# Optimization experiments

Measured on AMD Instinct MI355X. Metric: run time of the kernel, lower is better.

## Reference

```python
import jax, jax.numpy as jnp
import numpy as np
from jax import lax
from jax.scipy.linalg import solve_triangular

SR = 16000
FRAME_PERIOD = 80
FFT_LENGTH = 1024
WIN_MS = 30
EPS = 1e-05
DEFAULT_F0 = 150.0
B, T, N = 8, 320000, 4000

N_BAND = int(np.log2(SR / 600))  # 4
CUTOFF = [SR / 2 ** i for i in range(2, N_BAND + 1)]
CUTOFF.append(CUTOFF[-1])  # [4000, 2000, 1000, 1000]
SEG = [int(c * WIN_MS / 500 + 1.5) for c in CUTOFF]  # [241, 121, 61, 61]

_HHP_VALS = [0.00041447996898231424, 0.0007812505141729248, -0.0010917236836275842,
             -0.001986792567596759, 0.0020903896961562292, 0.004094057027284935,
             -0.0034025808529816698, -0.007496154127205602, 0.004972263339933064,
             0.012738791249119802, -0.006696032689574911, -0.020694051570247052,
             0.008432436565041345, 0.03307438375870053, -0.010018936738799522,
             -0.05423136140580825, 0.011293988915051487, 0.10020081367388213,
             -0.012120546202484579, -0.316300210390957, 0.5124068258062764]
_HLP_VALS = [-0.0006548817007748305, 7.561994958159384e-05, 0.0020408456937895227,
             -0.0007468053532203044, -0.004350223568826493, 0.0025966428382642732,
             0.007639602282756696, -0.006490411890149785, -0.011765804538954506,
             0.013649908479276255, 0.01636866479016021, -0.026075976030529347,
             -0.020910294856659444, 0.04826072503231665, 0.02476784661104811,
             -0.09617846758336064, -0.027359756709866623, 0.3148805216163004,
             0.5282734359405503]

def _qmf_high():
    h = np.zeros(41)
    h[:21] = _HHP_VALS
    h[21:] = h[19::-1]
    return h.astype(np.float32)

def _qmf_low():
    h = np.zeros(37)
    h[:19] = _HLP_VALS
    h[19:] = h[17::-1]
    return h.astype(np.float32)

def _make_window():
    w = np.zeros((N_BAND, SEG[0]), np.float32)
    for i, s in enumerate(SEG):
        w[i, :s] = np.hanning(s + 2)[1:-1]
    return w

def _interp_tables():
    coarse = np.concatenate([[0.0], [SR / 2 ** i for i in range(N_BAND, 0, -1)]])
    freq = np.arange(FFT_LENGTH // 2 + 1) * (SR / FFT_LENGTH)
    idx = np.clip(np.searchsorted(coarse, freq) - 1, 0, len(coarse) - 2)
    x0 = coarse[:-1]
    dx = coarse[1:] - x0
    wts = ((freq - x0[idx]) / dx[idx]).astype(np.float32)
    return idx.astype(np.int32), wts

_HHP = _qmf_high()
_HLP = _qmf_low()
_WIN = _make_window()
_IDX, _WTS = _interp_tables()


def _qmf_conv(x, h):
    # x: (B, T), h: (k,). Reflection pad k//2, cross-correlation, stride 2.
    p = h.shape[0] // 2
    xp = jnp.pad(x, ((0, 0), (p, p)), mode='reflect')
    out = lax.conv_general_dilated(xp[:, None, :], h[None, None, :], (2,), 'VALID',
                                   dimension_numbers=('NCH', 'OIH', 'NCH'))
    return out[:, 0, :]


def setup_inputs() -> dict:
    key = jax.random.key(0)
    k1, k2 = jax.random.split(key)
    x = jax.random.normal(k1, (B, T), jnp.float32)
    f0 = 100.0 + 200.0 * jax.random.uniform(k2, (B, N), jnp.float32)  # 100-300 Hz
    return {"x": x, "f0": f0}


def reference(x, f0):
    hHP = jnp.asarray(_HHP)
    hLP = jnp.asarray(_HLP)
    f0 = lax.stop_gradient(jnp.where(f0 <= 32, DEFAULT_F0, f0))
    Bn, Nf = f0.shape
    time_axis = jnp.arange(Nf, dtype=f0.dtype) * (FRAME_PERIOD / SR)
    bidx = jnp.arange(Bn)[:, None, None]
    eye6 = EPS * jnp.eye(6, dtype=x.dtype)
    lx = x
    bap = []
    for i in range(N_BAND):
        if i < N_BAND - 1:
            hx = _qmf_conv(lx, hHP)
            lx = _qmf_conv(lx, hLP)
            xb = hx
        else:
            xb = lx
        seg = SEG[i]
        tmp_fs = 2.0 * CUTOFF[i]
        pitch = tmp_fs / f0
        t0 = (pitch + 0.5).astype(jnp.int32)
        index_bias = (pitch * 0.5 + 0.5).astype(jnp.int32)
        curr_pos = (time_axis * tmp_fs + 1.5).astype(jnp.int32)[None, :]
        origin = curr_pos - index_bias  # (B, N)
        j = jnp.arange(-1, seg + 1)  # (seg+2,)
        T1 = xb.shape[-1] - 1
        ia = jnp.clip((origin - t0)[..., None] + j, 0, T1)
        ib = jnp.clip((origin + t0)[..., None] + j, 0, T1)
        Ha = xb[bidx, ia]  # (B, N, seg+2)
        Hb = xb[bidx, ib]

        def unfold3(a):  # size-3 sliding windows -> (B, N, seg, 3)
            return jnp.stack([a[..., 0:seg], a[..., 1:seg + 1], a[..., 2:seg + 2]], axis=-1)

        H = jnp.concatenate([unfold3(Ha), unfold3(Hb)], axis=-1)  # (B, N, seg, 6)
        w = jnp.asarray(_WIN[i, :seg])
        Hw = jnp.swapaxes(H, -2, -1) * w  # (B, N, 6, seg)
        R = Hw @ H  # (B, N, 6, 6)
        ig = jnp.clip(origin[..., None] + j[1:-1], 0, T1)
        X = xb[bidx, ig][..., None]  # (B, N, seg, 1)
        L = jnp.linalg.cholesky(R + eye6)
        b = Hw @ X  # (B, N, 6, 1)
        y1 = solve_triangular(L, b, lower=True)
        a = solve_triangular(jnp.swapaxes(L, -2, -1), y1, lower=False)
        HaX = H @ a  # (B, N, seg, 1)
        wsqrt = jnp.sqrt(w)
        wx = wsqrt * X[..., 0]
        wxHa = wsqrt * (X - HaX)[..., 0]
        A = jnp.std(wxHa, axis=-1, ddof=1) / (jnp.std(wx, axis=-1, ddof=1) + 1e-16)
        bap.append(A)
    bap.append(bap[-1])
    ap = jnp.stack(bap[::-1], axis=-1)  # (B, N, n_band+1), low->high freq
    # piecewise-linear interpolation in log domain onto fft bins
    y = jnp.log(ap)
    y0 = y[..., :-1]
    dy = y[..., 1:] - y0
    yi = jnp.take(dy, jnp.asarray(_IDX), axis=-1) * jnp.asarray(_WTS) \
         + jnp.take(y0, jnp.asarray(_IDX), axis=-1)
    return jnp.exp(yi)  # (B, N, fft//2+1)
```

## Files before the change

### kernel.cpp

```cpp
#include <hip/hip_runtime.h>
#include <math.h>

#define NB 8
#define NF 4000
#define NFRAMES (NB * NF)
#define TOTF (4 * NFRAMES)

__constant__ float c_hhp[21] = {
    0.00041447996898231424, 0.0007812505141729248, -0.0010917236836275842,
    -0.001986792567596759,  0.0020903896961562292, 0.004094057027284935,
    -0.0034025808529816698, -0.007496154127205602, 0.004972263339933064,
    0.012738791249119802,   -0.006696032689574911, -0.020694051570247052,
    0.008432436565041345,   0.03307438375870053,   -0.010018936738799522,
    -0.05423136140580825,   0.011293988915051487,  0.10020081367388213,
    -0.012120546202484579,  -0.316300210390957,    0.5124068258062764};
__constant__ float c_hlp[19] = {
    -0.0006548817007748305, 7.561994958159384e-05, 0.0020408456937895227,
    -0.0007468053532203044, -0.004350223568826493, 0.0025966428382642732,
    0.007639602282756696,   -0.006490411890149785, -0.011765804538954506,
    0.013649908479276255,   0.01636866479016021,   -0.026075976030529347,
    -0.020910294856659444,  0.04826072503231665,   0.02476784661104811,
    -0.09617846758336064,   -0.027359756709866623, 0.3148805216163004,
    0.5282734359405503};

__device__ __forceinline__ int reflidx(int i, int len) {
  if (i < 0) i = -i;
  if (i >= len) i = 2 * len - 2 - i;
  return i;
}
__device__ __forceinline__ int clampi(int i, int hi) {
  return min(max(i, 0), hi);
}
__device__ __forceinline__ float4 ld4(const float* p) {
  return *reinterpret_cast<const float4*>(p);
}
__device__ __forceinline__ void st4(float* p, float4 v) {
  *reinterpret_cast<float4*>(p) = v;
}

__global__ __launch_bounds__(256) void qmf_kernel(
    const float* __restrict__ in, int len, float* __restrict__ outH,
    float* __restrict__ outL, float2* __restrict__ wtab) {
  int half = len >> 1;
  int gid = blockIdx.x * 256 + threadIdx.x;
  if (gid >= NB * half) {
    if (wtab) {
      const int segs[4] = {241, 121, 61, 61};
      int k = threadIdx.x;
      for (int i = 0; i < 4; ++i) {
        float v = 0.f;
        if (k < segs[i]) {
          double ang = 2.0 * 3.14159265358979323846 * (double)(k + 1) /
                       (double)(segs[i] + 1);
          v = (float)(0.5 - 0.5 * cos(ang));
        }
        wtab[i * 256 + k] = make_float2(v, sqrtf(v));
      }
    }
    return;
  }
  int b = gid / half;
  int nn = gid - b * half;
  const float* row = in + (size_t)b * len;
  int c = 2 * nn;
  float sh = 0.f, sl = 0.f;
  if (c >= 20 && c <= len - 22) {
    const float2* p2 = reinterpret_cast<const float2*>(row + (c - 20));
    float v[42];
#pragma unroll
    for (int j = 0; j < 21; ++j) {
      float2 t = p2[j];
      v[2 * j] = t.x;
      v[2 * j + 1] = t.y;
    }
#pragma unroll
    for (int t = 0; t < 41; ++t) sh += v[t] * c_hhp[t <= 20 ? t : 40 - t];
#pragma unroll
    for (int t = 0; t < 37; ++t) sl += v[t + 2] * c_hlp[t <= 18 ? t : 36 - t];
  } else {
#pragma unroll
    for (int t = 0; t < 41; ++t)
      sh += row[reflidx(c + t - 20, len)] * c_hhp[t <= 20 ? t : 40 - t];
#pragma unroll
    for (int t = 0; t < 37; ++t)
      sl += row[reflidx(c + t - 18, len)] * c_hlp[t <= 18 ? t : 36 - t];
  }
  outH[(size_t)b * half + nn] = sh;
  outL[(size_t)b * half + nn] = sl;
}

__device__ __forceinline__ void accum1(float wk, float wsk, float h0, float h1,
                                       float h2, float h3, float h4, float h5,
                                       float x, float* __restrict__ rr,
                                       float* __restrict__ bv,
                                       float* __restrict__ gv, float& sxx,
                                       float& s1x) {
  sxx += wk * x * x;
  s1x += wsk * x;
  float wh0 = wk * h0, wh1 = wk * h1, wh2 = wk * h2, wh3 = wk * h3,
        wh4 = wk * h4, wh5 = wk * h5;
  gv[0] += wsk * h0; gv[1] += wsk * h1; gv[2] += wsk * h2;
  gv[3] += wsk * h3; gv[4] += wsk * h4; gv[5] += wsk * h5;
  bv[0] += wh0 * x;  bv[1] += wh1 * x;  bv[2] += wh2 * x;
  bv[3] += wh3 * x;  bv[4] += wh4 * x;  bv[5] += wh5 * x;
  rr[0] += wh0 * h0;  rr[1] += wh0 * h1;  rr[2] += wh0 * h2;
  rr[3] += wh0 * h3;  rr[4] += wh0 * h4;  rr[5] += wh0 * h5;
  rr[6] += wh1 * h1;  rr[7] += wh1 * h2;  rr[8] += wh1 * h3;
  rr[9] += wh1 * h4;  rr[10] += wh1 * h5; rr[11] += wh2 * h2;
  rr[12] += wh2 * h3; rr[13] += wh2 * h4; rr[14] += wh2 * h5;
  rr[15] += wh3 * h3; rr[16] += wh3 * h4; rr[17] += wh3 * h5;
  rr[18] += wh4 * h4; rr[19] += wh4 * h5; rr[20] += wh5 * h5;
}

template <int GS, int NITER, bool CLAMP>
__device__ __forceinline__ void acc_loop(
    const float* __restrict__ row, int T1, int base_a, int base_b, int origin,
    int sub, const float2* __restrict__ wtab, float rr[21], float bv[6],
    float gv[6], float& sxx, float& s1x) {
  if (!CLAMP) {
    const float* pa = row + base_a + 4 * sub;
    const float* pb = row + base_b + 4 * sub;
    const float* pg = row + origin + 4 * sub;
    const float* pw = reinterpret_cast<const float*>(wtab + 4 * sub);
#pragma unroll 2
    for (int j = 0; j < NITER; ++j) {
      const int off = j * 4 * GS;
      float4 a0 = ld4(pa + off);
      float4 a1 = ld4(pa + off + 4);
      float4 b0 = ld4(pb + off);
      float4 b1 = ld4(pb + off + 4);
      float4 xx = ld4(pg + off);
      float4 w01 = ld4(pw + 2 * off);
      float4 w23 = ld4(pw + 2 * off + 4);
      accum1(w01.x, w01.y, a0.x, a0.y, a0.z, b0.x, b0.y, b0.z, xx.x, rr, bv,
             gv, sxx, s1x);
      accum1(w01.z, w01.w, a0.y, a0.z, a0.w, b0.y, b0.z, b0.w, xx.y, rr, bv,
             gv, sxx, s1x);
      accum1(w23.x, w23.y, a0.z, a0.w, a1.x, b0.z, b0.w, b1.x, xx.z, rr, bv,
             gv, sxx, s1x);
      accum1(w23.z, w23.w, a0.w, a1.x, a1.y, b0.w, b1.x, b1.y, xx.w, rr, bv,
             gv, sxx, s1x);
    }
  } else {
#pragma unroll 2
    for (int j = 0; j < NITER; ++j) {
#pragma unroll
      for (int m = 0; m < 4; ++m) {
        int k = 4 * (sub + j * GS) + m;
        float2 wp = wtab[k];
        int ia = base_a + k, ib = base_b + k;
        float h0 = row[clampi(ia, T1)];
        float h1 = row[clampi(ia + 1, T1)];
        float h2 = row[clampi(ia + 2, T1)];
        float h3 = row[clampi(ib, T1)];
        float h4 = row[clampi(ib + 1, T1)];
        float h5 = row[clampi(ib + 2, T1)];
        float x = row[clampi(origin + k, T1)];
        accum1(wp.x, wp.y, h0, h1, h2, h3, h4, h5, x, rr, bv, gv, sxx, s1x);
      }
    }
  }
}

template <int SEG, int LGS, int NITER>
__device__ __forceinline__ void band_body(
    const float* __restrict__ xb, int bandLen, const float* __restrict__ f0,
    float tmp_fs, const float2* __restrict__ wtab, float* __restrict__ sums_col,
    int blk) {
  constexpr int GS = 1 << LGS;
  constexpr int FPB = 256 / GS;
  constexpr int KMAX = 4 * GS * NITER;
  const int tid = threadIdx.x;
  const int sub = tid & (GS - 1);
  const int frame = blk * FPB + (tid >> LGS);
  const int b = frame / NF;
  const int n = frame - b * NF;

  float f0v = f0[frame];
  if (f0v <= 32.0f) f0v = 150.0f;
  float pitch = tmp_fs / f0v;
  int t0 = (int)(__fadd_rn(pitch, 0.5f));
  int ibias = (int)(__fadd_rn(__fmul_rn(pitch, 0.5f), 0.5f));
  float tt = __fmul_rn((float)n, 0.005f);
  int curr = (int)(__fadd_rn(__fmul_rn(tt, tmp_fs), 1.5f));
  int origin = curr - ibias;
  const int T1 = bandLen - 1;
  const float* row = xb + (size_t)b * bandLen;
  const int base_a = origin - t0 - 1;
  const int base_b = origin + t0 - 1;

  float rr[21], bv[6], gv[6], sxx = 0.f, s1x = 0.f;
#pragma unroll
  for (int i = 0; i < 21; ++i) rr[i] = 0.f;
#pragma unroll
  for (int i = 0; i < 6; ++i) bv[i] = 0.f;
#pragma unroll
  for (int i = 0; i < 6; ++i) gv[i] = 0.f;

  const bool fast = (base_a >= 0) && (base_b + KMAX + 3 <= T1);
  if (fast)
    acc_loop<GS, NITER, false>(row, T1, base_a, base_b, origin, sub, wtab, rr,
                               bv, gv, sxx, s1x);
  else
    acc_loop<GS, NITER, true>(row, T1, base_a, base_b, origin, sub, wtab, rr,
                              bv, gv, sxx, s1x);

#pragma unroll
  for (int off = GS / 2; off >= 1; off >>= 1) {
#pragma unroll
    for (int i = 0; i < 21; ++i) rr[i] += __shfl_xor(rr[i], off, 64);
#pragma unroll
    for (int i = 0; i < 6; ++i) bv[i] += __shfl_xor(bv[i], off, 64);
#pragma unroll
    for (int i = 0; i < 6; ++i) gv[i] += __shfl_xor(gv[i], off, 64);
    sxx += __shfl_xor(sxx, off, 64);
    s1x += __shfl_xor(s1x, off, 64);
  }

  if (sub == 0) {
    float* sp = sums_col + frame;
#pragma unroll
    for (int i = 0; i < 21; ++i) sp[(size_t)i * TOTF] = rr[i];
#pragma unroll
    for (int i = 0; i < 6; ++i) sp[(size_t)(21 + i) * TOTF] = bv[i];
#pragma unroll
    for (int i = 0; i < 6; ++i) sp[(size_t)(27 + i) * TOTF] = gv[i];
    sp[(size_t)33 * TOTF] = sxx;
    sp[(size_t)34 * TOTF] = s1x;
  }
}

__global__ __launch_bounds__(256) void bands_kernel(
    const float* __restrict__ hx0, const float* __restrict__ hx1,
    const float* __restrict__ hx2, const float* __restrict__ lx2,
    const float* __restrict__ f0, const float2* __restrict__ wtab,
    float* __restrict__ sums) {
  int blk = blockIdx.x;
  if (blk < 2000) {
    band_body<241, 4, 4>(hx0, 160000, f0, 8000.0f, wtab + 0 * 256,
                         sums + 0 * NFRAMES, blk);
  } else if (blk < 3000) {
    band_body<121, 3, 4>(hx1, 80000, f0, 4000.0f, wtab + 1 * 256,
                         sums + 1 * NFRAMES, blk - 2000);
  } else if (blk < 3500) {
    band_body<61, 2, 4>(hx2, 40000, f0, 2000.0f, wtab + 2 * 256,
                        sums + 2 * NFRAMES, blk - 3000);
  } else {
    band_body<61, 2, 4>(lx2, 40000, f0, 2000.0f, wtab + 3 * 256,
                        sums + 3 * NFRAMES, blk - 3500);
  }
}

__global__ __launch_bounds__(256) void solve_kernel(
    const float* __restrict__ sums, float* __restrict__ Aarr) {
  const int t = blockIdx.x * 256 + threadIdx.x;
  float v[35];
#pragma unroll
  for (int i = 0; i < 35; ++i) v[i] = sums[(size_t)i * TOTF + t];
  const float nf = (t >= 2 * NFRAMES) ? 61.0f
                   : (t >= NFRAMES)   ? 121.0f
                                      : 241.0f;
  float sxx = v[33], s1x = v[34];

  float M[6][6], invd[6];
  {
    int c = 0;
#pragma unroll
    for (int p = 0; p < 6; ++p)
#pragma unroll
      for (int q = p; q < 6; ++q) {
        M[p][q] = v[c];
        M[q][p] = v[c];
        ++c;
      }
#pragma unroll
    for (int p = 0; p < 6; ++p) M[p][p] += 1e-5f;
  }
#pragma unroll
  for (int p = 0; p < 6; ++p) {
    float d = M[p][p];
#pragma unroll
    for (int j = 0; j < 6; ++j)
      if (j < p) d -= M[p][j] * M[p][j];
    d = sqrtf(d);
    M[p][p] = d;
    float inv = 1.0f / d;
    invd[p] = inv;
#pragma unroll
    for (int q = 0; q < 6; ++q)
      if (q > p) {
        float s = M[q][p];
#pragma unroll
        for (int j = 0; j < 6; ++j)
          if (j < p) s -= M[q][j] * M[p][j];
        M[q][p] = s * inv;
      }
  }
  float yv[6], av[6];
#pragma unroll
  for (int p = 0; p < 6; ++p) {
    float s = v[21 + p];
#pragma unroll
    for (int j = 0; j < 6; ++j)
      if (j < p) s -= M[p][j] * yv[j];
    yv[p] = s * invd[p];
  }
#pragma unroll
  for (int p = 5; p >= 0; --p) {
    float s = yv[p];
#pragma unroll
    for (int j = 0; j < 6; ++j)
      if (j > p) s -= M[j][p] * av[j];
    av[p] = s * invd[p];
  }

  float adotb = 0.f, adotg = 0.f, quad = 0.f;
  {
    int c = 0;
#pragma unroll
    for (int p = 0; p < 6; ++p) {
      adotb += av[p] * v[21 + p];
      adotg += av[p] * v[27 + p];
#pragma unroll
      for (int q = p; q < 6; ++q) {
        float tt = av[p] * av[q] * v[c++];
        quad += (q == p) ? tt : 2.f * tt;
      }
    }
  }
  float s2r = sxx - 2.f * adotb + quad;
  float s1r = s1x - adotg;
  float vx = (sxx - s1x * s1x / nf) / (nf - 1.0f);
  float vr = (s2r - s1r * s1r / nf) / (nf - 1.0f);
  float sx = sqrtf(fmaxf(vx, 0.f));
  float sr = sqrtf(fmaxf(vr, 0.f));
  Aarr[t] = sr / (sx + 1e-16f);
}

__global__ __launch_bounds__(256) void interp_kernel(
    const float* __restrict__ A, float* __restrict__ out) {
  const int wave = threadIdx.x >> 6;
  const int lane = threadIdx.x & 63;
  const int f = blockIdx.x * 4 + wave;
  float l0 = __logf(A[0 * NFRAMES + f]);
  float l1 = __logf(A[1 * NFRAMES + f]);
  float l2 = __logf(A[2 * NFRAMES + f]);
  float l3 = __logf(A[3 * NFRAMES + f]);
  float d1 = l2 - l3, d2 = l1 - l2, d3 = l0 - l1;
  float* orow = out + (size_t)f * 513;
  float vals[8];
#pragma unroll
  for (int m = 0; m < 8; ++m) {
    int k = 8 * lane + m;
    float y0, dy, c;
    int k0;
    if (k <= 64) {
      y0 = l3; dy = 0.f; k0 = 0; c = 0.015625f;
    } else if (k <= 128) {
      y0 = l3; dy = d1; k0 = 64; c = 0.015625f;
    } else if (k <= 256) {
      y0 = l2; dy = d2; k0 = 128; c = 0.0078125f;
    } else {
      y0 = l1; dy = d3; k0 = 256; c = 0.00390625f;
    }
    float w = (float)(k - k0) * c;
    vals[m] = __expf(y0 + w * dy);
  }
  st4(orow + 8 * lane, make_float4(vals[0], vals[1], vals[2], vals[3]));
  st4(orow + 8 * lane + 4, make_float4(vals[4], vals[5], vals[6], vals[7]));
  if (lane == 0) orow[512] = __expf(l1 + d3);
}

extern "C" void kernel_launch(void* const* d_in, const int* in_sizes, int n_in,
                              void* d_out, int out_size, void* d_ws,
                              size_t ws_size, hipStream_t stream) {
  const float* x = (const float*)d_in[0];
  const float* f0 = (const float*)d_in[1];
  float* out = (float*)d_out;
  float* ws = (float*)d_ws;

  float* hx0 = ws + 0;
  float* lx0 = hx0 + 1280000;
  float* hx1 = lx0 + 1280000;
  float* lx1 = hx1 + 640000;
  float* hx2 = lx1 + 640000;
  float* lx2 = hx2 + 320000;
  float* Aarr = lx2 + 320000;
  float2* wtab = (float2*)(Aarr + 4 * NFRAMES);
  float* sums = (float*)(wtab + 4 * 256);
  (void)ws_size;

  hipLaunchKernelGGL(qmf_kernel, dim3(5000), dim3(256), 0, stream, x, 320000,
                     hx0, lx0, (float2*)nullptr);
  hipLaunchKernelGGL(qmf_kernel, dim3(2500), dim3(256), 0, stream, lx0,
                     160000, hx1, lx1, (float2*)nullptr);
  hipLaunchKernelGGL(qmf_kernel, dim3(1251), dim3(256), 0, stream, lx1, 80000,
                     hx2, lx2, wtab);

  hipLaunchKernelGGL(bands_kernel, dim3(4000), dim3(256), 0, stream, hx0, hx1,
                     hx2, lx2, f0, wtab, sums);

  hipLaunchKernelGGL(solve_kernel, dim3(TOTF / 256), dim3(256), 0, stream,
                     sums, Aarr);

  hipLaunchKernelGGL(interp_kernel, dim3(NFRAMES / 4), dim3(256), 0, stream,
                     Aarr, out);
}
```

Measured before the change: 86.07 us.

## Co-schedule band statistics with next QMF level and fuse solve into interp

Each band's statistics kernel now runs in the same launch as the next QMF decomposition level, so independent work overlaps inside one grid instead of running in separate serial launches. Band template parameters (frames per block, split) change for each band. The 6x6 Cholesky solve is folded into the interpolation kernel: 16 threads per block compute log-aperiodicity into LDS, which removes one launch and the Aarr round trip. The risks are load imbalance between the heterogeneous block types and only 16 active threads during the solve phase of each interp block.

Result: slower. 111.6 us (+29.7%).

```diff
diff --git a/kernel.cpp b/kernel.cpp
--- a/kernel.cpp
+++ b/kernel.cpp
@@ -38,27 +38,11 @@
   *reinterpret_cast<float4*>(p) = v;
 }
 
-__global__ __launch_bounds__(256) void qmf_kernel(
-    const float* __restrict__ in, int len, float* __restrict__ outH,
-    float* __restrict__ outL, float2* __restrict__ wtab) {
+__device__ __forceinline__ void qmf_body(const float* __restrict__ in, int len,
+                                         float* __restrict__ outH,
+                                         float* __restrict__ outL, int gid) {
   int half = len >> 1;
-  int gid = blockIdx.x * 256 + threadIdx.x;
-  if (gid >= NB * half) {
-    if (wtab) {
-      const int segs[4] = {241, 121, 61, 61};
-      int k = threadIdx.x;
-      for (int i = 0; i < 4; ++i) {
-        float v = 0.f;
-        if (k < segs[i]) {
-          double ang = 2.0 * 3.14159265358979323846 * (double)(k + 1) /
-                       (double)(segs[i] + 1);
-          v = (float)(0.5 - 0.5 * cos(ang));
-        }
-        wtab[i * 256 + k] = make_float2(v, sqrtf(v));
-      }
-    }
-    return;
-  }
+  if (gid >= NB * half) return;
   int b = gid / half;
   int nn = gid - b * half;
   const float* row = in + (size_t)b * len;
@@ -87,6 +71,27 @@
   }
   outH[(size_t)b * half + nn] = sh;
   outL[(size_t)b * half + nn] = sl;
+}
+
+__global__ __launch_bounds__(256) void qmf0_kernel(
+    const float* __restrict__ in, float* __restrict__ outH,
+    float* __restrict__ outL, float2* __restrict__ wtab) {
+  int gid = blockIdx.x * 256 + threadIdx.x;
+  if (gid >= NB * 160000) {
+    const int segs[4] = {241, 121, 61, 61};
+    int k = threadIdx.x;
+    for (int i = 0; i < 4; ++i) {
+      float v = 0.f;
+      if (k < segs[i]) {
+        double ang = 2.0 * 3.14159265358979323846 * (double)(k + 1) /
+                     (double)(segs[i] + 1);
+        v = (float)(0.5 - 0.5 * cos(ang));
+      }
+      wtab[i * 256 + k] = make_float2(v, sqrtf(v));
+    }
+    return;
+  }
+  qmf_body(in, 320000, outH, outL, gid);
 }
 
 __device__ __forceinline__ void accum1(float wk, float wsk, float h0, float h1,
@@ -230,122 +235,146 @@
   }
 }
 
-__global__ __launch_bounds__(256) void bands_kernel(
-    const float* __restrict__ hx0, const float* __restrict__ hx1,
+__global__ __launch_bounds__(256) void band0_qmf1_kernel(
+    const float* __restrict__ lx0, float* __restrict__ hx1,
+    float* __restrict__ lx1, const float* __restrict__ hx0,
+    const float* __restrict__ f0, const float2* __restrict__ wtab,
+    float* __restrict__ sums) {
+  int blk = blockIdx.x;
+  if (blk < 1000) {
+    band_body<241, 3, 8>(hx0, 160000, f0, 8000.0f, wtab + 0 * 256,
+                         sums + 0 * NFRAMES, blk);
+  } else {
+    qmf_body(lx0, 160000, hx1, lx1, (blk - 1000) * 256 + threadIdx.x);
+  }
+}
+
+__global__ __launch_bounds__(256) void band1_qmf2_kernel(
+    const float* __restrict__ lx1, float* __restrict__ hx2,
+    float* __restrict__ lx2, const float* __restrict__ hx1,
+    const float* __restrict__ f0, const float2* __restrict__ wtab,
+    float* __restrict__ sums) {
+  int blk = blockIdx.x;
+  if (blk < 1000) {
+    band_body<121, 3, 4>(hx1, 80000, f0, 4000.0f, wtab + 1 * 256,
+                         sums + 1 * NFRAMES, blk);
+  } else {
+    qmf_body(lx1, 80000, hx2, lx2, (blk - 1000) * 256 + threadIdx.x);
+  }
+}
+
+__global__ __launch_bounds__(256) void bands23_kernel(
     const float* __restrict__ hx2, const float* __restrict__ lx2,
     const float* __restrict__ f0, const float2* __restrict__ wtab,
     float* __restrict__ sums) {
   int blk = blockIdx.x;
-  if (blk < 2000) {
-    band_body<241, 4, 4>(hx0, 160000, f0, 8000.0f, wtab + 0 * 256,
-                         sums + 0 * NFRAMES, blk);
-  } else if (blk < 3000) {
-    band_body<121, 3, 4>(hx1, 80000, f0, 4000.0f, wtab + 1 * 256,
-                         sums + 1 * NFRAMES, blk - 2000);
-  } else if (blk < 3500) {
-    band_body<61, 2, 4>(hx2, 40000, f0, 2000.0f, wtab + 2 * 256,
-                        sums + 2 * NFRAMES, blk - 3000);
+  if (blk < 1000) {
+    band_body<61, 3, 2>(hx2, 40000, f0, 2000.0f, wtab + 2 * 256,
+                        sums + 2 * NFRAMES, blk);
   } else {
-    band_body<61, 2, 4>(lx2, 40000, f0, 2000.0f, wtab + 3 * 256,
-                        sums + 3 * NFRAMES, blk - 3500);
-  }
-}
-
-__global__ __launch_bounds__(256) void solve_kernel(
-    const float* __restrict__ sums, float* __restrict__ Aarr) {
-  const int t = blockIdx.x * 256 + threadIdx.x;
-  float v[35];
-#pragma unroll
-  for (int i = 0; i < 35; ++i) v[i] = sums[(size_t)i * TOTF + t];
-  const float nf = (t >= 2 * NFRAMES) ? 61.0f
-                   : (t >= NFRAMES)   ? 121.0f
-                                      : 241.0f;
-  float sxx = v[33], s1x = v[34];
-
-  float M[6][6], invd[6];
-  {
-    int c = 0;
-#pragma unroll
-    for (int p = 0; p < 6; ++p)
-#pragma unroll
-      for (int q = p; q < 6; ++q) {
-        M[p][q] = v[c];
-        M[q][p] = v[c];
-        ++c;
+    band_body<61, 3, 2>(lx2, 40000, f0, 2000.0f, wtab + 3 * 256,
+                        sums + 3 * NFRAMES, blk - 1000);
+  }
+}
+
+__global__ __launch_bounds__(256) void solve_interp_kernel(
+    const float* __restrict__ sums, float* __restrict__ out) {
+  __shared__ float lds_l[16];
+  const int tid = threadIdx.x;
+  const int blk = blockIdx.x;
+  if (tid < 16) {
+    const int band = tid >> 2;
+    const int fl = tid & 3;
+    const int col = band * NFRAMES + blk * 4 + fl;
+    float v[35];
+#pragma unroll
+    for (int i = 0; i < 35; ++i) v[i] = sums[(size_t)i * TOTF + col];
+    const float nf = (band >= 2) ? 61.0f : (band == 1 ? 121.0f : 241.0f);
+    float sxx = v[33], s1x = v[34];
+
+    float M[6][6], invd[6];
+    {
+      int c = 0;
+#pragma unroll
+      for (int p = 0; p < 6; ++p)
+#pragma unroll
+        for (int q = p; q < 6; ++q) {
+          M[p][q] = v[c];
+          M[q][p] = v[c];
+          ++c;
+        }
+#pragma unroll
+      for (int p = 0; p < 6; ++p) M[p][p] += 1e-5f;
+    }
+#pragma unroll
+    for (int p = 0; p < 6; ++p) {
+      float d = M[p][p];
+#pragma unroll
+      for (int j = 0; j < 6; ++j)
+        if (j < p) d -= M[p][j] * M[p][j];
+      d = sqrtf(d);
+      M[p][p] = d;
+      float inv = 1.0f / d;
+      invd[p] = inv;
+#pragma unroll
+      for (int q = 0; q < 6; ++q)
+        if (q > p) {
+          float s = M[q][p];
+#pragma unroll
+          for (int j = 0; j < 6; ++j)
+            if (j < p) s -= M[q][j] * M[p][j];
+          M[q][p] = s * inv;
+        }
+    }
+    float yv[6], av[6];
+#pragma unroll
+    for (int p = 0; p < 6; ++p) {
+      float s = v[21 + p];
+#pragma unroll
+      for (int j = 0; j < 6; ++j)
+        if (j < p) s -= M[p][j] * yv[j];
+      yv[p] = s * invd[p];
+    }
+#pragma unroll
+    for (int p = 5; p >= 0; --p) {
+      float s = yv[p];
+#pragma unroll
+      for (int j = 0; j < 6; ++j)
+        if (j > p) s -= M[j][p] * av[j];
+      av[p] = s * invd[p];
+    }
+
+    float adotb = 0.f, adotg = 0.f, quad = 0.f;
+    {
+      int c = 0;
+#pragma unroll
+      for (int p = 0; p < 6; ++p) {
+        adotb += av[p] * v[21 + p];
+        adotg += av[p] * v[27 + p];
+#pragma unroll
+        for (int q = p; q < 6; ++q) {
+          float tt = av[p] * av[q] * v[c++];
+          quad += (q == p) ? tt : 2.f * tt;
+        }
       }
-#pragma unroll
-    for (int p = 0; p < 6; ++p) M[p][p] += 1e-5f;
-  }
-#pragma unroll
-  for (int p = 0; p < 6; ++p) {
-    float d = M[p][p];
-#pragma unroll
-    for (int j = 0; j < 6; ++j)
-      if (j < p) d -= M[p][j] * M[p][j];
-    d = sqrtf(d);
-    M[p][p] = d;
-    float inv = 1.0f / d;
-    invd[p] = inv;
-#pragma unroll
-    for (int q = 0; q < 6; ++q)
-      if (q > p) {
-        float s = M[q][p];
-#pragma unroll
-        for (int j = 0; j < 6; ++j)
-          if (j < p) s -= M[q][j] * M[p][j];
-        M[q][p] = s * inv;
-      }
-  }
-  float yv[6], av[6];
-#pragma unroll
-  for (int p = 0; p < 6; ++p) {
-    float s = v[21 + p];
-#pragma unroll
-    for (int j = 0; j < 6; ++j)
-      if (j < p) s -= M[p][j] * yv[j];
-    yv[p] = s * invd[p];
-  }
-#pragma unroll
-  for (int p = 5; p >= 0; --p) {
-    float s = yv[p];
-#pragma unroll
-    for (int j = 0; j < 6; ++j)
-      if (j > p) s -= M[j][p] * av[j];
-    av[p] = s * invd[p];
-  }
-
-  float adotb = 0.f, adotg = 0.f, quad = 0.f;
-  {
-    int c = 0;
-#pragma unroll
-    for (int p = 0; p < 6; ++p) {
-      adotb += av[p] * v[21 + p];
-      adotg += av[p] * v[27 + p];
-#pragma unroll
-      for (int q = p; q < 6; ++q) {
-        float tt = av[p] * av[q] * v[c++];
-        quad += (q == p) ? tt : 2.f * tt;
-      }
-    }
-  }
-  float s2r = sxx - 2.f * adotb + quad;
-  float s1r = s1x - adotg;
-  float vx = (sxx - s1x * s1x / nf) / (nf - 1.0f);
-  float vr = (s2r - s1r * s1r / nf) / (nf - 1.0f);
-  float sx = sqrtf(fmaxf(vx, 0.f));
-  float sr = sqrtf(fmaxf(vr, 0.f));
-  Aarr[t] = sr / (sx + 1e-16f);
-}
-
-__global__ __launch_bounds__(256) void interp_kernel(
-    const float* __restrict__ A, float* __restrict__ out) {
-  const int wave = threadIdx.x >> 6;
-  const int lane = threadIdx.x & 63;
-  const int f = blockIdx.x * 4 + wave;
-  float l0 = __logf(A[0 * NFRAMES + f]);
-  float l1 = __logf(A[1 * NFRAMES + f]);
-  float l2 = __logf(A[2 * NFRAMES + f]);
-  float l3 = __logf(A[3 * NFRAMES + f]);
+    }
+    float s2r = sxx - 2.f * adotb + quad;
+    float s1r = s1x - adotg;
+    float vx = (sxx - s1x * s1x / nf) / (nf - 1.0f);
+    float vr = (s2r - s1r * s1r / nf) / (nf - 1.0f);
+    float sx = sqrtf(fmaxf(vx, 0.f));
+    float sr = sqrtf(fmaxf(vr, 0.f));
+    lds_l[fl * 4 + band] = __logf(sr / (sx + 1e-16f));
+  }
+  __syncthreads();
+
+  const int wave = tid >> 6;
+  const int lane = tid & 63;
+  const int f = blk * 4 + wave;
+  float l0 = lds_l[wave * 4 + 0];
+  float l1 = lds_l[wave * 4 + 1];
+  float l2 = lds_l[wave * 4 + 2];
+  float l3 = lds_l[wave * 4 + 3];
   float d1 = l2 - l3, d2 = l1 - l2, d3 = l0 - l1;
   float* orow = out + (size_t)f * 513;
   float vals[8];
@@ -385,24 +414,18 @@
   float* lx1 = hx1 + 640000;
   float* hx2 = lx1 + 640000;
   float* lx2 = hx2 + 320000;
-  float* Aarr = lx2 + 320000;
-  float2* wtab = (float2*)(Aarr + 4 * NFRAMES);
+  float2* wtab = (float2*)(lx2 + 320000);
   float* sums = (float*)(wtab + 4 * 256);
   (void)ws_size;
 
-  hipLaunchKernelGGL(qmf_kernel, dim3(5000), dim3(256), 0, stream, x, 320000,
-                     hx0, lx0, (float2*)nullptr);
-  hipLaunchKernelGGL(qmf_kernel, dim3(2500), dim3(256), 0, stream, lx0,
-                     160000, hx1, lx1, (float2*)nullptr);
-  hipLaunchKernelGGL(qmf_kernel, dim3(1251), dim3(256), 0, stream, lx1, 80000,
-                     hx2, lx2, wtab);
-
-  hipLaunchKernelGGL(bands_kernel, dim3(4000), dim3(256), 0, stream, hx0, hx1,
-                     hx2, lx2, f0, wtab, sums);
-
-  hipLaunchKernelGGL(solve_kernel, dim3(TOTF / 256), dim3(256), 0, stream,
-                     sums, Aarr);
-
-  hipLaunchKernelGGL(interp_kernel, dim3(NFRAMES / 4), dim3(256), 0, stream,
-                     Aarr, out);
-}
+  hipLaunchKernelGGL(qmf0_kernel, dim3(5001), dim3(256), 0, stream, x, hx0,
+                     lx0, wtab);
+  hipLaunchKernelGGL(band0_qmf1_kernel, dim3(3500), dim3(256), 0, stream, lx0,
+                     hx1, lx1, hx0, f0, wtab, sums);
+  hipLaunchKernelGGL(band1_qmf2_kernel, dim3(2250), dim3(256), 0, stream, lx1,
+                     hx2, lx2, hx1, f0, wtab, sums);
+  hipLaunchKernelGGL(bands23_kernel, dim3(2000), dim3(256), 0, stream, hx2,
+                     lx2, f0, wtab, sums);
+  hipLaunchKernelGGL(solve_interp_kernel, dim3(NFRAMES / 4), dim3(256), 0,
+                     stream, sums, out);
+}
```
